# Performance work log

Hardware: AMD Instinct MI355X
Metric: run time of the kernel (lower is better)

Reference implementation:

```python
import jax, jax.numpy as jnp
import numpy as np

H = 48       # query heads
KVH = 8      # kv heads (GQA)
G = H // KVH # groups = 6
D = 128      # head_dim
HID = 6144
ROPE_THETA = 1e6


def setup_inputs() -> dict:
    key = jax.random.key(0)
    k1, k2, k3 = jax.random.split(key, 3)
    x = jax.random.normal(k1, (2, 2048, HID), dtype=jnp.float32)
    Wqkv = jax.random.normal(k2, (8192, HID), dtype=jnp.float32) * 0.02
    Wo = jax.random.normal(k3, (HID, HID), dtype=jnp.float32) * 0.02
    return {"x": x, "Wqkv": Wqkv, "Wo": Wo}


def _rotate_half(u):
    return jnp.concatenate([-u[..., D // 2:], u[..., :D // 2]], axis=-1)


def reference(x, Wqkv, Wo):
    B, S, _ = x.shape
    # fused QKV projection, InternLM2 packed layout [B,S,KVH,2+G,D]
    qkv = jnp.einsum('bsh,oh->bso', x, Wqkv).reshape(B, S, KVH, G + 2, D)
    q = qkv[..., :G, :].reshape(B, S, H, D)   # [B,S,H,D]
    k = qkv[..., G, :]                        # [B,S,KVH,D]
    v = qkv[..., G + 1, :]                    # [B,S,KVH,D]

    # RoPE (rotate-half style, theta=1e6)
    inv_freq = 1.0 / (ROPE_THETA ** (jnp.arange(0, D, 2, dtype=jnp.float32) / D))
    freqs = jnp.outer(jnp.arange(S, dtype=jnp.float32), inv_freq)  # [S, D/2]
    emb = jnp.concatenate([freqs, freqs], axis=-1)                 # [S, D]
    cos = jnp.cos(emb)[None, :, None, :]
    sin = jnp.sin(emb)[None, :, None, :]
    q = q * cos + _rotate_half(q) * sin
    k = k * cos + _rotate_half(k) * sin

    # GQA: expand kv heads to query heads
    k = jnp.repeat(k, G, axis=2)  # [B,S,H,D]
    v = jnp.repeat(v, G, axis=2)

    scale = jnp.float32(1.0 / np.sqrt(D))
    scores = jnp.einsum('bqhd,bkhd->bhqk', q, k) * scale  # [B,H,S,S]
    causal = jnp.tril(jnp.ones((S, S), dtype=bool))
    scores = jnp.where(causal[None, None], scores, jnp.float32(-1e30))
    attn = jax.nn.softmax(scores, axis=-1)
    ctx = jnp.einsum('bhqk,bkhd->bqhd', attn, v).reshape(B, S, HID)
    return jnp.einsum('bsh,oh->bso', ctx, Wo)
```

## Files before the change

kernel.cpp:

```cpp
#include <hip/hip_runtime.h>
#include <stdint.h>
#include <stddef.h>


typedef unsigned short u16;
typedef __attribute__((ext_vector_type(8))) short short8;
typedef __attribute__((ext_vector_type(4))) float f32x4;
typedef __attribute__((ext_vector_type(4))) unsigned short u16x4;

typedef const __attribute__((address_space(1))) void* as1_cvp;
typedef __attribute__((address_space(3))) void* as3_vp;

__device__ __forceinline__ float bf2f(u16 u) {
  union { unsigned int i; float f; } v; v.i = ((unsigned)u) << 16; return v.f;
}
__device__ __forceinline__ u16 f2bf(float f) {
  union { float f; unsigned int i; } v; v.f = f;
  unsigned r = v.i + 0x7FFFu + ((v.i >> 16) & 1u);
  return (u16)(r >> 16);
}
__device__ __forceinline__ void gload_lds16(const void* g, void* l) {
  __builtin_amdgcn_global_load_lds((as1_cvp)g, (as3_vp)l, 16, 0, 0);
}

__global__ __launch_bounds__(256) void k_f2bf(const float* __restrict__ in,
                                              u16* __restrict__ out) {
  size_t i = ((size_t)blockIdx.x * 256 + threadIdx.x) * 4;
  f32x4 v = *(const f32x4*)(in + i);
  u16x4 o;
  o[0] = f2bf(v[0]); o[1] = f2bf(v[1]); o[2] = f2bf(v[2]); o[3] = f2bf(v[3]);
  *(u16x4*)(out + i) = o;
}

template<int WRITE_BF16>
__global__ __launch_bounds__(256) void k_gemm_bt(const u16* __restrict__ A,
                                                 const u16* __restrict__ B,
                                                 void* __restrict__ Cout,
                                                 int M, int N, int K) {
  __shared__ u16 As[128][64];
  __shared__ u16 Bs[128][64];
  const int tid  = threadIdx.x;
  const int lane = tid & 63;
  const int w    = tid >> 6;
  const int wr   = w >> 1, wc = w & 1;
  const int l16  = lane & 15, lhi = lane >> 4;
  const int srow = lane >> 3;
  const int scol = ((lane & 7) ^ (lane >> 3)) * 8;
  const int swz  = (l16 & 7) << 3;

  const int nbx = gridDim.x;
  int id = blockIdx.y * nbx + blockIdx.x;
  const int cpx = (nbx * gridDim.y) >> 3;
  id = (id & 7) * cpx + (id >> 3);
  const long m0 = (long)(id / nbx) * 128;
  const long n0 = (long)(id % nbx) * 128;

  f32x4 acc[4][4] = {};

  const u16* Ap = A + (size_t)m0 * K + scol;
  const u16* Bp = B + (size_t)n0 * K + scol;
  const int kTiles = K >> 6;
  for (int kt = 0; kt < kTiles; ++kt) {
    const int kb = kt << 6;
    #pragma unroll
    for (int c = 0; c < 4; ++c) {
      const int rr = (w * 4 + c) * 8 + srow;
      gload_lds16(Ap + (size_t)rr * K + kb, &As[(w * 4 + c) * 8][0]);
      gload_lds16(Bp + (size_t)rr * K + kb, &Bs[(w * 4 + c) * 8][0]);
    }
    __syncthreads();
    #pragma unroll
    for (int kk = 0; kk < 64; kk += 32) {
      short8 af[4], bfr[4];
      #pragma unroll
      for (int mi = 0; mi < 4; ++mi)
        af[mi] = *(const short8*)&As[wr * 64 + mi * 16 + l16][(kk + lhi * 8) ^ swz];
      #pragma unroll
      for (int ni = 0; ni < 4; ++ni)
        bfr[ni] = *(const short8*)&Bs[wc * 64 + ni * 16 + l16][(kk + lhi * 8) ^ swz];
      #pragma unroll
      for (int mi = 0; mi < 4; ++mi)
        #pragma unroll
        for (int ni = 0; ni < 4; ++ni)
          acc[mi][ni] = __builtin_amdgcn_mfma_f32_16x16x32_bf16(
              af[mi], bfr[ni], acc[mi][ni], 0, 0, 0);
    }
    __syncthreads();
  }
  #pragma unroll
  for (int mi = 0; mi < 4; ++mi)
    #pragma unroll
    for (int ni = 0; ni < 4; ++ni)
      #pragma unroll
      for (int j = 0; j < 4; ++j) {
        const size_t row = m0 + wr * 64 + mi * 16 + lhi * 4 + j;
        const size_t col = n0 + wc * 64 + ni * 16 + l16;
        const float v = acc[mi][ni][j];
        if (WRITE_BF16) ((u16*)Cout)[row * N + col] = f2bf(v);
        else            ((float*)Cout)[row * N + col] = v;
      }
}

__global__ __launch_bounds__(256) void k_rope(const u16* __restrict__ QKV,
                                              u16* __restrict__ Qo,
                                              u16* __restrict__ Ko) {
  const unsigned tid = blockIdx.x * 256 + threadIdx.x;
  const int j    = tid & 63;
  const int slot = (tid >> 6) & 7;
  const int kvh  = (tid >> 9) & 7;
  const int t    = tid >> 12;
  if (slot == 7) return;
  const int b = t >> 11, s = t & 2047;
  const size_t base = (size_t)t * 8192 + kvh * 1024 + slot * 128;
  const float v0 = bf2f(QKV[base + j]);
  const float v1 = bf2f(QKV[base + j + 64]);
  const float invf = __expf(-(float)j * 0.21586735246819181f);
  const float ang = (float)s * invf;
  float sn, cs;
  __sincosf(ang, &sn, &cs);
  const float o0 = v0 * cs - v1 * sn;
  const float o1 = v1 * cs + v0 * sn;
  if (slot < 6) {
    const int hh = kvh * 6 + slot;
    const size_t o = ((size_t)(b * 48 + hh) * 2048 + s) * 128 + j;
    Qo[o] = f2bf(o0); Qo[o + 64] = f2bf(o1);
  } else {
    const size_t o = ((size_t)(b * 8 + kvh) * 2048 + s) * 128 + j;
    Ko[o] = f2bf(o0); Ko[o + 64] = f2bf(o1);
  }
}

__global__ __launch_bounds__(256) void k_vtrans(const u16* __restrict__ QKV,
                                                u16* __restrict__ VT) {
  __shared__ u16 T[64][136];
  const int bid = blockIdx.x;
  const int st  = bid & 31;
  const int kvh = (bid >> 5) & 7;
  const int b   = bid >> 8;
  const int tid = threadIdx.x;
  const int r   = tid >> 4;
  const int c8  = (tid & 15) * 8;
  const size_t qoff = ((size_t)(b * 2048 + st * 64)) * 8192 + kvh * 1024 + 896;
  #pragma unroll
  for (int p = 0; p < 4; ++p) {
    short8 v = *(const short8*)&QKV[qoff + (size_t)(p * 16 + r) * 8192 + c8];
    *(short8*)&T[p * 16 + r][c8] = v;
  }
  __syncthreads();
  const int dd = tid >> 3;
  const int s8 = (tid & 7) * 8;
  const size_t vbase = ((size_t)(b * 8 + kvh) * 128) * 2048 + st * 64;
  #pragma unroll
  for (int p = 0; p < 4; ++p) {
    const int d = p * 32 + dd;
    short8 o;
    #pragma unroll
    for (int i = 0; i < 8; ++i) o[i] = (short)T[s8 + i][d];
    *(short8*)&VT[vbase + (size_t)d * 2048 + s8] = o;
  }
}

__global__ __launch_bounds__(256) void k_attn(const u16* __restrict__ Q,
                                              const u16* __restrict__ Kg,
                                              const u16* __restrict__ VT,
                                              u16* __restrict__ CTX) {
  __shared__ u16 Ks[64][128];
  __shared__ u16 Vs[128][64];
  __shared__ u16 Ps[4][16][64];
  const int bid = blockIdx.x;
  const int qt  = 31 - (bid / 96);
  const int bh  = bid % 96;
  const int h   = bh % 48;
  const int b   = bh / 48;
  const int kvh = h / 6;
  const int tid = threadIdx.x, lane = tid & 63, w = tid >> 6;
  const int l16 = lane & 15, lhi = lane >> 4;
  const int swz = (l16 & 7) << 3;
  const float SC = 0.08838834764831845f;

  short8 qf[4];
  {
    const size_t qrow = ((size_t)(b * 48 + h) * 2048 + qt * 64 + w * 16 + l16) * 128;
    #pragma unroll
    for (int kc = 0; kc < 4; ++kc)
      qf[kc] = *(const short8*)&Q[qrow + kc * 32 + lhi * 8];
  }
  f32x4 cacc[8] = {};
  float m_r[4], l_r[4];
  #pragma unroll
  for (int j = 0; j < 4; ++j) { m_r[j] = -1e30f; l_r[j] = 0.f; }

  const u16* Kb = Kg + (size_t)(b * 8 + kvh) * 2048 * 128;
  const u16* Vb = VT + (size_t)(b * 8 + kvh) * 128 * 2048;

  for (int kt = 0; kt <= qt; ++kt) {
    #pragma unroll
    for (int c = 0; c < 4; ++c) {
      const int krow = w * 16 + c * 4 + lhi;
      const int kcol = (l16 * 8) ^ ((krow & 7) << 3);
      gload_lds16(&Kb[(size_t)(kt * 64 + krow) * 128 + kcol], &Ks[w * 16 + c * 4][0]);
      const int vrow = w * 32 + c * 8 + (lane >> 3);
      const int vcol = ((lane & 7) * 8) ^ (((lane >> 3) & 7) << 3);
      gload_lds16(&Vb[(size_t)vrow * 2048 + kt * 64 + vcol], &Vs[w * 32 + c * 8][0]);
    }
    __syncthreads();

    f32x4 sacc[4] = {};
    #pragma unroll
    for (int ni = 0; ni < 4; ++ni)
      #pragma unroll
      for (int kc = 0; kc < 4; ++kc) {
        const short8 kfr = *(const short8*)&Ks[ni * 16 + l16][(kc * 32 + lhi * 8) ^ swz];
        sacc[ni] = __builtin_amdgcn_mfma_f32_16x16x32_bf16(qf[kc], kfr, sacc[ni], 0, 0, 0);
      }

    const bool diag = (kt == qt);
    float sv[4][4], alpha[4];
    #pragma unroll
    for (int j = 0; j < 4; ++j) {
      const int rloc = w * 16 + lhi * 4 + j;
      float mx = -1e30f;
      #pragma unroll
      for (int ni = 0; ni < 4; ++ni) {
        float s = sacc[ni][j] * SC;
        if (diag && (ni * 16 + l16 > rloc)) s = -1e30f;
        sv[ni][j] = s;
        mx = fmaxf(mx, s);
      }
      mx = fmaxf(mx, __shfl_xor(mx, 1, 16));
      mx = fmaxf(mx, __shfl_xor(mx, 2, 16));
      mx = fmaxf(mx, __shfl_xor(mx, 4, 16));
      mx = fmaxf(mx, __shfl_xor(mx, 8, 16));
      const float mnew = fmaxf(m_r[j], mx);
      alpha[j] = __expf(m_r[j] - mnew);
      float rs = 0.f;
      #pragma unroll
      for (int ni = 0; ni < 4; ++ni) {
        const float p = __expf(sv[ni][j] - mnew);
        sv[ni][j] = p;
        rs += p;
      }
      rs += __shfl_xor(rs, 1, 16);
      rs += __shfl_xor(rs, 2, 16);
      rs += __shfl_xor(rs, 4, 16);
      rs += __shfl_xor(rs, 8, 16);
      l_r[j] = l_r[j] * alpha[j] + rs;
      m_r[j] = mnew;
    }
    #pragma unroll
    for (int ni = 0; ni < 4; ++ni)
      #pragma unroll
      for (int j = 0; j < 4; ++j)
        Ps[w][lhi * 4 + j][(ni * 16 + l16) ^ (((lhi * 4 + j) & 7) << 3)] = f2bf(sv[ni][j]);
    #pragma unroll
    for (int nb = 0; nb < 8; ++nb)
      #pragma unroll
      for (int j = 0; j < 4; ++j)
        cacc[nb][j] *= alpha[j];
    #pragma unroll
    for (int kc2 = 0; kc2 < 2; ++kc2) {
      const short8 pa = *(const short8*)&Ps[w][l16][(kc2 * 32 + lhi * 8) ^ swz];
      #pragma unroll
      for (int nb = 0; nb < 8; ++nb) {
        const short8 vfr = *(const short8*)&Vs[nb * 16 + l16][(kc2 * 32 + lhi * 8) ^ swz];
        cacc[nb] = __builtin_amdgcn_mfma_f32_16x16x32_bf16(pa, vfr, cacc[nb], 0, 0, 0);
      }
    }
    __syncthreads();
  }

  const size_t crow = (size_t)(b * 2048 + qt * 64 + w * 16);
  #pragma unroll
  for (int nb = 0; nb < 8; ++nb)
    #pragma unroll
    for (int j = 0; j < 4; ++j) {
      const float v = cacc[nb][j] / l_r[j];
      CTX[(crow + lhi * 4 + j) * 6144 + h * 128 + nb * 16 + l16] = f2bf(v);
    }
}

extern "C" void kernel_launch(void* const* d_in, const int* in_sizes, int n_in,
                              void* d_out, int out_size, void* d_ws, size_t ws_size,
                              hipStream_t stream) {
  const float* x    = (const float*)d_in[0];
  const float* wqkv = (const float*)d_in[1];
  const float* wo   = (const float*)d_in[2];
  float* out = (float*)d_out;
  char* ws = (char*)d_ws;

  u16* xb  = (u16*)(ws);
  u16* wqb = (u16*)(ws + 50331648UL);
  u16* wob = (u16*)(ws + 150994944UL);
  u16* qkv = (u16*)(ws + 226492416UL);
  u16* Qb  = (u16*)(ws + 293601280UL);
  u16* Kb  = (u16*)(ws + 343932928UL);
  u16* VTb = (u16*)(ws + 352321536UL);
  u16* ctx = (u16*)(ws + 360710144UL);

  k_f2bf<<<25165824 / 1024, 256, 0, stream>>>(x, xb);
  k_f2bf<<<50331648 / 1024, 256, 0, stream>>>(wqkv, wqb);
  k_f2bf<<<37748736 / 1024, 256, 0, stream>>>(wo, wob);

  k_gemm_bt<1><<<dim3(8192 / 128, 4096 / 128), 256, 0, stream>>>(
      xb, wqb, qkv, 4096, 8192, 6144);

  k_rope<<<16777216 / 256, 256, 0, stream>>>(qkv, Qb, Kb);
  k_vtrans<<<512, 256, 0, stream>>>(qkv, VTb);

  k_attn<<<2 * 48 * 32, 256, 0, stream>>>(Qb, Kb, VTb, ctx);

  k_gemm_bt<0><<<dim3(6144 / 128, 4096 / 128), 256, 0, stream>>>(
      ctx, wob, out, 4096, 6144, 6144);
}
```

Baseline: 1.301 ms.

## Replace GEMM with 256x256 double-buffered, ping-pong scheduled 8-wave kernel

Measured after the change: 1.207 ms. 1.08x faster.

```diff
diff --git a/kernel.cpp b/kernel.cpp
--- a/kernel.cpp
+++ b/kernel.cpp
@@ -32,70 +32,144 @@
   *(u16x4*)(out + i) = o;
 }
 
+__device__ __forceinline__ void stage_region(const u16* __restrict__ G,
+                                             int K, int kt,
+                                             u16 (* __restrict__ XS)[64],
+                                             int rmap, int w, int lane) {
+  #pragma unroll
+  for (int L = 0; L < 2; ++L) {
+    const int g = w * 2 + L;
+    int rb;
+    if (rmap == 0)      rb = g * 8 + (g >> 3) * 64;
+    else if (rmap == 1) rb = 64 + g * 8 + (g >> 3) * 64;
+    else if (rmap == 2) rb = (g >> 2) * 64 + (g & 3) * 8;
+    else                rb = 32 + (g >> 2) * 64 + (g & 3) * 8;
+    const int srow = rb + (lane >> 3);
+    const int schunk = ((lane & 7) ^ ((lane >> 3) & 7)) * 8;
+    gload_lds16(G + (size_t)srow * K + (size_t)kt * 64 + schunk, &XS[rb][0]);
+  }
+}
+
+#define LDFRAG(XS, row, ks) \
+  (*(const short8*)&XS[row][(((ks) * 32) + lhi * 8) ^ swz])
+
+#define MFMA_Q(af, bf, mb, nb)                                              \
+  _Pragma("unroll") for (int mf = 0; mf < 4; ++mf)                          \
+  _Pragma("unroll") for (int nf = 0; nf < 2; ++nf)                          \
+  _Pragma("unroll") for (int ks = 0; ks < 2; ++ks)                          \
+    acc[(mb) + mf][(nb) + nf] = __builtin_amdgcn_mfma_f32_16x16x32_bf16(    \
+        af[mf][ks], bf[nf][ks], acc[(mb) + mf][(nb) + nf], 0, 0, 0);
+
+#define GEMM_HALF(H) {                                                      \
+  const int tAhi  = (t + 1 + (H) < nkt) ? (t + 1 + (H)) : (nkt - 1);        \
+  const int tNext = (t + 2 + (H) < nkt) ? (t + 2 + (H)) : (nkt - 1);        \
+  short8 a0[4][2], a1[4][2], b0[2][2], b1[2][2];                            \
+                         \
+  _Pragma("unroll") for (int mf = 0; mf < 4; ++mf) {                        \
+    a0[mf][0] = LDFRAG(As[H], wm * 128 + mf * 16 + l16, 0);                 \
+    a0[mf][1] = LDFRAG(As[H], wm * 128 + mf * 16 + l16, 1); }               \
+  _Pragma("unroll") for (int nf = 0; nf < 2; ++nf) {                        \
+    b0[nf][0] = LDFRAG(Bs[H], wn * 64 + nf * 16 + l16, 0);                  \
+    b0[nf][1] = LDFRAG(Bs[H], wn * 64 + nf * 16 + l16, 1); }                \
+  stage_region(Ap, K, tAhi, As[1 - (H)], 1, w, lane);                       \
+  asm volatile("s_waitcnt lgkmcnt(8)" ::: "memory");                        \
+  __builtin_amdgcn_s_barrier();                                             \
+  asm volatile("s_waitcnt lgkmcnt(0)" ::: "memory");                        \
+  __builtin_amdgcn_sched_barrier(0);                                        \
+  __builtin_amdgcn_s_setprio(1);                                            \
+  MFMA_Q(a0, b0, 0, 0);                                                     \
+  __builtin_amdgcn_s_setprio(0);                                            \
+  __builtin_amdgcn_s_barrier();                                             \
+                          \
+  _Pragma("unroll") for (int nf = 0; nf < 2; ++nf) {                        \
+    b1[nf][0] = LDFRAG(Bs[H], wn * 64 + (nf + 2) * 16 + l16, 0);            \
+    b1[nf][1] = LDFRAG(Bs[H], wn * 64 + (nf + 2) * 16 + l16, 1); }          \
+  stage_region(Ap, K, tNext, As[H], 0, w, lane);                            \
+  __builtin_amdgcn_s_barrier();                                             \
+  asm volatile("s_waitcnt lgkmcnt(0)" ::: "memory");                        \
+  __builtin_amdgcn_sched_barrier(0);                                        \
+  __builtin_amdgcn_s_setprio(1);                                            \
+  MFMA_Q(a0, b1, 0, 2);                                                     \
+  __builtin_amdgcn_s_setprio(0);                                            \
+  __builtin_amdgcn_s_barrier();                                             \
+                          \
+  _Pragma("unroll") for (int mf = 0; mf < 4; ++mf) {                        \
+    a1[mf][0] = LDFRAG(As[H], wm * 128 + (mf + 4) * 16 + l16, 0);           \
+    a1[mf][1] = LDFRAG(As[H], wm * 128 + (mf + 4) * 16 + l16, 1); }         \
+  stage_region(Bp, K, tNext, Bs[H], 2, w, lane);                            \
+  __builtin_amdgcn_s_barrier();                                             \
+  asm volatile("s_waitcnt lgkmcnt(0)" ::: "memory");                        \
+  __builtin_amdgcn_sched_barrier(0);                                        \
+  __builtin_amdgcn_s_setprio(1);                                            \
+  MFMA_Q(a1, b0, 4, 0);                                                     \
+  __builtin_amdgcn_s_setprio(0);                                            \
+  __builtin_amdgcn_s_barrier();                                             \
+      \
+  stage_region(Bp, K, tNext, Bs[H], 3, w, lane);                            \
+  asm volatile("s_waitcnt vmcnt(6)" ::: "memory");                          \
+  __builtin_amdgcn_s_barrier();                                             \
+  __builtin_amdgcn_s_setprio(1);                                            \
+  MFMA_Q(a1, b1, 4, 2);                                                     \
+  __builtin_amdgcn_s_setprio(0);                                            \
+  __builtin_amdgcn_s_barrier();                                             \
+}
+
 template<int WRITE_BF16>
-__global__ __launch_bounds__(256) void k_gemm_bt(const u16* __restrict__ A,
-                                                 const u16* __restrict__ B,
-                                                 void* __restrict__ Cout,
-                                                 int M, int N, int K) {
-  __shared__ u16 As[128][64];
-  __shared__ u16 Bs[128][64];
+__global__ __launch_bounds__(512, 2) void k_gemm256(const u16* __restrict__ A,
+                                                    const u16* __restrict__ B,
+                                                    void* __restrict__ Cout,
+                                                    int M, int N, int K) {
+  __shared__ u16 As[2][256][64];
+  __shared__ u16 Bs[2][256][64];
+  (void)M;
   const int tid  = threadIdx.x;
   const int lane = tid & 63;
   const int w    = tid >> 6;
-  const int wr   = w >> 1, wc = w & 1;
+  const int wm   = w >> 2;
+  const int wn   = w & 3;
   const int l16  = lane & 15, lhi = lane >> 4;
-  const int srow = lane >> 3;
-  const int scol = ((lane & 7) ^ (lane >> 3)) * 8;
   const int swz  = (l16 & 7) << 3;
 
   const int nbx = gridDim.x;
   int id = blockIdx.y * nbx + blockIdx.x;
   const int cpx = (nbx * gridDim.y) >> 3;
   id = (id & 7) * cpx + (id >> 3);
-  const long m0 = (long)(id / nbx) * 128;
-  const long n0 = (long)(id % nbx) * 128;
-
-  f32x4 acc[4][4] = {};
-
-  const u16* Ap = A + (size_t)m0 * K + scol;
-  const u16* Bp = B + (size_t)n0 * K + scol;
-  const int kTiles = K >> 6;
-  for (int kt = 0; kt < kTiles; ++kt) {
-    const int kb = kt << 6;
-    #pragma unroll
-    for (int c = 0; c < 4; ++c) {
-      const int rr = (w * 4 + c) * 8 + srow;
-      gload_lds16(Ap + (size_t)rr * K + kb, &As[(w * 4 + c) * 8][0]);
-      gload_lds16(Bp + (size_t)rr * K + kb, &Bs[(w * 4 + c) * 8][0]);
-    }
-    __syncthreads();
-    #pragma unroll
-    for (int kk = 0; kk < 64; kk += 32) {
-      short8 af[4], bfr[4];
-      #pragma unroll
-      for (int mi = 0; mi < 4; ++mi)
-        af[mi] = *(const short8*)&As[wr * 64 + mi * 16 + l16][(kk + lhi * 8) ^ swz];
-      #pragma unroll
-      for (int ni = 0; ni < 4; ++ni)
-        bfr[ni] = *(const short8*)&Bs[wc * 64 + ni * 16 + l16][(kk + lhi * 8) ^ swz];
-      #pragma unroll
-      for (int mi = 0; mi < 4; ++mi)
-        #pragma unroll
-        for (int ni = 0; ni < 4; ++ni)
-          acc[mi][ni] = __builtin_amdgcn_mfma_f32_16x16x32_bf16(
-              af[mi], bfr[ni], acc[mi][ni], 0, 0, 0);
-    }
-    __syncthreads();
-  }
-  #pragma unroll
-  for (int mi = 0; mi < 4; ++mi)
-    #pragma unroll
-    for (int ni = 0; ni < 4; ++ni)
+  const long m0 = (long)(id / nbx) * 256;
+  const long n0 = (long)(id % nbx) * 256;
+
+  const u16* Ap = A + (size_t)m0 * K;
+  const u16* Bp = B + (size_t)n0 * K;
+
+  f32x4 acc[8][4] = {};
+  const int nkt = K >> 6;
+  const int niter = nkt >> 1;
+
+  stage_region(Ap, K, 0, As[0], 0, w, lane);
+  stage_region(Ap, K, 0, As[0], 1, w, lane);
+  stage_region(Bp, K, 0, Bs[0], 2, w, lane);
+  stage_region(Bp, K, 0, Bs[0], 3, w, lane);
+  stage_region(Ap, K, 1, As[1], 0, w, lane);
+  stage_region(Bp, K, 1, Bs[1], 2, w, lane);
+  stage_region(Bp, K, 1, Bs[1], 3, w, lane);
+  asm volatile("s_waitcnt vmcnt(6)" ::: "memory");
+  __builtin_amdgcn_s_barrier();
+
+  for (int i = 0; i < niter; ++i) {
+    const int t = 2 * i;
+    GEMM_HALF(0)
+    GEMM_HALF(1)
+  }
+
+  asm volatile("s_waitcnt vmcnt(0)" ::: "memory");
+  #pragma unroll
+  for (int mf = 0; mf < 8; ++mf)
+    #pragma unroll
+    for (int nf = 0; nf < 4; ++nf)
       #pragma unroll
       for (int j = 0; j < 4; ++j) {
-        const size_t row = m0 + wr * 64 + mi * 16 + lhi * 4 + j;
-        const size_t col = n0 + wc * 64 + ni * 16 + l16;
-        const float v = acc[mi][ni][j];
+        const size_t row = m0 + wm * 128 + mf * 16 + lhi * 4 + j;
+        const size_t col = n0 + wn * 64 + nf * 16 + l16;
+        const float v = acc[mf][nf][j];
         if (WRITE_BF16) ((u16*)Cout)[row * N + col] = f2bf(v);
         else            ((float*)Cout)[row * N + col] = v;
       }
@@ -301,7 +375,7 @@
   k_f2bf<<<50331648 / 1024, 256, 0, stream>>>(wqkv, wqb);
   k_f2bf<<<37748736 / 1024, 256, 0, stream>>>(wo, wob);
 
-  k_gemm_bt<1><<<dim3(8192 / 128, 4096 / 128), 256, 0, stream>>>(
+  k_gemm256<1><<<dim3(8192 / 256, 4096 / 256), 512, 0, stream>>>(
       xb, wqb, qkv, 4096, 8192, 6144);
 
   k_rope<<<16777216 / 256, 256, 0, stream>>>(qkv, Qb, Kb);
@@ -309,6 +383,6 @@
 
   k_attn<<<2 * 48 * 32, 256, 0, stream>>>(Qb, Kb, VTb, ctx);
 
-  k_gemm_bt<0><<<dim3(6144 / 128, 4096 / 128), 256, 0, stream>>>(
+  k_gemm256<0><<<dim3(6144 / 256, 4096 / 256), 512, 0, stream>>>(
       ctx, wob, out, 4096, 6144, 6144);
 }
```
